# Kernel tuning notes

Measured on AMD Instinct MI355X. Metric: run time of the kernel, lower is better.

## Reference

```python
import jax, jax.numpy as jnp
import numpy as np

COUNT_PRIOR_LOG_ODDS = -2.0  # frozen value of exponential_decay(**cfg.OBJ_PRES_COUNT_LOG_PRIOR)
EPS = 1e-9                   # safe_log epsilon
B, H, W = 1024, 16, 16


def setup_inputs() -> dict:
    key = jax.random.key(0)
    k1, k2 = jax.random.split(key)
    z_pres = jax.random.uniform(k1, (B, 1, H, W), dtype=jnp.float32)
    z_pres_prob = jax.random.uniform(k2, (B, 1, H, W), dtype=jnp.float32)
    return {"z_pres": z_pres, "z_pres_prob": z_pres_prob}


def _safe_log(x):
    return jnp.log(x + EPS)


def reference(z_pres, z_pres_prob):
    b, _, h, w = z_pres.shape
    hw = h * w
    s = hw + 1  # count support size

    count_support = jnp.arange(s, dtype=jnp.float32)  # [S]
    p = 1.0 / (jnp.exp(jnp.float32(-COUNT_PRIOR_LOG_ODDS)) + 1.0)
    cd0 = (1.0 - p) * p ** count_support
    cd0 = cd0 / cd0.sum()
    cd0 = jnp.broadcast_to(cd0[None, :], (b, s))      # count_distribution [B, S]
    csf0 = jnp.zeros((b, 1), jnp.float32)             # count_so_far [B, 1]

    # flatten grid in row-major (h, w) order to scan axis: [HW, B, 1]
    probs = z_pres_prob.reshape(b, 1, hw).transpose(2, 0, 1)
    pres = z_pres.reshape(b, 1, hw).transpose(2, 0, 1)
    steps = jnp.arange(hw, dtype=jnp.float32)

    def step(carry, xs):
        cd, csf = carry                 # [B, S], [B, 1]
        prob, zp, i = xs                # [B, 1], [B, 1], scalar
        denom = hw - i
        # P(z=1 | C, z_prev): clamp(count_support - count_so_far, 0, HW - i) / (HW - i)
        p_z_given = jnp.clip(count_support[None, :] - csf, 0.0, denom) / denom  # [B, S]
        p_z = jnp.sum(cd * p_z_given, axis=1, keepdims=True)                    # [B, 1] (the bmm)
        kl = (prob * (_safe_log(prob) - _safe_log(p_z))
              + (1.0 - prob) * (_safe_log(1.0 - prob) - _safe_log(1.0 - p_z)))
        sample = jnp.round(zp)                                                  # [B, 1]
        mult = sample * p_z_given + (1.0 - sample) * (1.0 - p_z_given)          # [B, S]
        cd1 = mult * cd
        norm = jnp.clip(jnp.sum(cd1, axis=1, keepdims=True), 1e-6, None)
        return (cd1 / norm, csf + sample), kl

    (_, _), kls = jax.lax.scan(step, (cd0, csf0), (probs, pres, steps))
    # kls: [HW, B, 1] -> obj_kl [B, 1, H, W]
    return kls.transpose(1, 2, 0).reshape(b, 1, h, w)
```

## Files before the change

kernel.cpp:

```cpp
#include <hip/hip_runtime.h>
#include <math.h>

#define HW 256
#define MINNORM 1.17549435e-38f


struct InvTbl { float v[HW]; };
static constexpr InvTbl make_inv() {
    InvTbl t{};
    for (int i = 0; i < HW; ++i) t.v[i] = 1.0f / (float)(HW - i);
    return t;
}
__constant__ InvTbl INVD = make_inv();

template <int CTRL>
__device__ __forceinline__ float dpp_sra(float x) {
    int s = __builtin_amdgcn_update_dpp(0, __builtin_bit_cast(int, x),
                                        CTRL, 0xf, 0xf, true);
    return x + __builtin_bit_cast(float, s);
}

__device__ __forceinline__ float rdlane(float x, int l) {
    return __builtin_bit_cast(float,
        __builtin_amdgcn_readlane(__builtin_bit_cast(int, x), l));
}

__device__ __forceinline__ float wave_total(float x) {
    x = dpp_sra<0x111>(x);
    x = dpp_sra<0x112>(x);
    x = dpp_sra<0x114>(x);
    x = dpp_sra<0x118>(x);
    const float a = rdlane(x, 15), b = rdlane(x, 31), c = rdlane(x, 47);
    return (a + b) + c;
}

__global__ void __launch_bounds__(64)
spair_count_kl(const float* __restrict__ z_pres,
               const float* __restrict__ z_prob,
               float* __restrict__ out) {
    float tok;
    asm volatile("s_setreg_imm32_b32 hwreg(HW_REG_MODE, 4, 2), 0\n\t"
                 "v_mov_b32 %0, 0" : "=v"(tok));

    const int lane = threadIdx.x;
    const int b = blockIdx.x;

    const float e2f = (float)exp(2.0);
    const float pf  = (float)(1.0 / ((double)e2f + 1.0));
    const double pd = (double)pf;
    const double l2p = log2(pd);
    float cd = 0.0f;
    if (lane <= 41) {
        const double powj = exp2((double)lane * l2p);
        float v = (float)((1.0 - pd) * powj);
        cd = (v < MINNORM) ? 0.0f : v;
    }
    {
        float s = cd;
#pragma unroll
        for (int off = 32; off > 0; off >>= 1) s += __shfl_xor(s, off, 64);
        cd = cd / s;
    }
    cd += tok;
    const float jf = (float)lane;
    float csf = tok;

    const float* presb = z_pres + (size_t)b * HW;
    const float* probb = z_prob + (size_t)b * HW;
    float* outb = out + (size_t)b * HW;

    bool dead = false;

#pragma unroll 1
    for (int k = 0; k < 4; ++k) {
        const float myprob = probb[k * 64 + lane];
        const float mypres = presb[k * 64 + lane];
        const unsigned long long smask = __ballot(rintf(mypres) != 0.0f);
        float my_pz = 0.0f;

        if (!dead) {
#pragma unroll 1
            for (int blk = 0; blk < 4; ++blk) {
                float p2 = 1.0f;
#pragma unroll
                for (int u = 0; u < 16; ++u) {
                    const int ii = blk * 16 + u;
                    const int i = k * 64 + ii;
                    const float fden = (float)(HW - i);
                    const float inv = INVD.v[i];
                    const bool s1 = ((smask >> ii) & 1ULL) != 0ULL;

                    const float t = fminf(fmaxf(jf - csf, 0.0f), fden);
                    const float pg = (t == fden) ? 1.0f : t * inv;
                    const float mult = s1 ? pg : (1.0f - pg);

                    const float prodm = cd * mult;
                    const float p1 = cd * pg;
                    p2 = wave_total(prodm);
                    const float p1s = wave_total(p1);
                    const float pz = s1 ? p2 : p1s;

                    const float norm = fmaxf(p2, 1e-6f);
                    cd = prodm * __builtin_amdgcn_rcpf(norm);
                    csf += s1 ? 1.0f : 0.0f;

                    my_pz = (ii == lane) ? pz : my_pz;
                }
                if (p2 == 0.0f) { dead = true; break; }
            }
        }

        const float prob = myprob;
        const float pz = my_pz;
        const float kl = prob * (logf(prob + 1e-9f) - logf(pz + 1e-9f))
                       + (1.0f - prob) * (logf((1.0f - prob) + 1e-9f)
                                        - logf((1.0f - pz) + 1e-9f));
        outb[k * 64 + lane] = kl;
    }
}

extern "C" void kernel_launch(void* const* d_in, const int* in_sizes, int n_in,
                              void* d_out, int out_size, void* d_ws, size_t ws_size,
                              hipStream_t stream) {
    const float* z_pres = (const float*)d_in[0];
    const float* z_prob = (const float*)d_in[1];
    float* out = (float*)d_out;
    const int nbatch = in_sizes[0] / HW;
    spair_count_kl<<<dim3(nbatch), dim3(64), 0, stream>>>(z_pres, z_prob, out);
}
```

Baseline: 69.36 us.

## Pack four batch rows per wave with 16-lane row reductions

Each wave now processes four batch elements, one per 16-lane row. Each lane holds three count-support entries, so the 42 nonzero entries fit in 48 slots. The cross-lane sums become row-local DPP butterflies that broadcast within the row, replacing the full-wave reduction that ended in readlanes, and the two sums are interleaved. This cuts the grid to a quarter of the waves and removes the scalar readlane serialization. In exchange, each lane does more work per step, and the early-exit check now waits until all four rows are dead.

```diff
diff --git a/kernel.cpp b/kernel.cpp
--- a/kernel.cpp
+++ b/kernel.cpp
@@ -14,24 +14,26 @@
 __constant__ InvTbl INVD = make_inv();
 
 template <int CTRL>
-__device__ __forceinline__ float dpp_sra(float x) {
+__device__ __forceinline__ float dpp_add(float x) {
     int s = __builtin_amdgcn_update_dpp(0, __builtin_bit_cast(int, x),
                                         CTRL, 0xf, 0xf, true);
     return x + __builtin_bit_cast(float, s);
 }
 
-__device__ __forceinline__ float rdlane(float x, int l) {
-    return __builtin_bit_cast(float,
-        __builtin_amdgcn_readlane(__builtin_bit_cast(int, x), l));
+__device__ __forceinline__ float rowsum_bcast(float x) {
+    x = dpp_add<0xB1>(x);
+    x = dpp_add<0x4E>(x);
+    x = dpp_add<0x124>(x);
+    x = dpp_add<0x128>(x);
+    return x;
 }
-
-__device__ __forceinline__ float wave_total(float x) {
-    x = dpp_sra<0x111>(x);
-    x = dpp_sra<0x112>(x);
-    x = dpp_sra<0x114>(x);
-    x = dpp_sra<0x118>(x);
-    const float a = rdlane(x, 15), b = rdlane(x, 31), c = rdlane(x, 47);
-    return (a + b) + c;
+__device__ __forceinline__ void rowsum_bcast2(float a, float z,
+                                              float& ra, float& rz) {
+    a = dpp_add<0xB1>(a);   z = dpp_add<0xB1>(z);
+    a = dpp_add<0x4E>(a);   z = dpp_add<0x4E>(z);
+    a = dpp_add<0x124>(a);  z = dpp_add<0x124>(z);
+    a = dpp_add<0x128>(a);  z = dpp_add<0x128>(z);
+    ra = a; rz = z;
 }
 
 __global__ void __launch_bounds__(64)
@@ -43,26 +45,32 @@
                  "v_mov_b32 %0, 0" : "=v"(tok));
 
     const int lane = threadIdx.x;
-    const int b = blockIdx.x;
+    const int c = lane & 15;
+    const int b = blockIdx.x * 4 + (lane >> 4);
 
     const float e2f = (float)exp(2.0);
     const float pf  = (float)(1.0 / ((double)e2f + 1.0));
     const double pd = (double)pf;
     const double l2p = log2(pd);
-    float cd = 0.0f;
-    if (lane <= 41) {
-        const double powj = exp2((double)lane * l2p);
-        float v = (float)((1.0 - pd) * powj);
-        cd = (v < MINNORM) ? 0.0f : v;
+    float cd[3], jf[3];
+#pragma unroll
+    for (int s = 0; s < 3; ++s) {
+        const int j = c + 16 * s;
+        jf[s] = (float)j;
+        float v = 0.0f;
+        if (j <= 41) {
+            const double powj = exp2((double)j * l2p);
+            float w = (float)((1.0 - pd) * powj);
+            v = (w < MINNORM) ? 0.0f : w;
+        }
+        cd[s] = v;
     }
     {
-        float s = cd;
+        const float part = (cd[0] + cd[1]) + cd[2];
+        const float rsum = rowsum_bcast(part);
 #pragma unroll
-        for (int off = 32; off > 0; off >>= 1) s += __shfl_xor(s, off, 64);
-        cd = cd / s;
+        for (int s = 0; s < 3; ++s) cd[s] = cd[s] / rsum + tok;
     }
-    cd += tok;
-    const float jf = (float)lane;
     float csf = tok;
 
     const float* presb = z_pres + (size_t)b * HW;
@@ -73,49 +81,69 @@
 
 #pragma unroll 1
     for (int k = 0; k < 4; ++k) {
-        const float myprob = probb[k * 64 + lane];
-        const float mypres = presb[k * 64 + lane];
-        const unsigned long long smask = __ballot(rintf(mypres) != 0.0f);
-        float my_pz = 0.0f;
+        float pres_q[4], prob_q[4];
+#pragma unroll
+        for (int q = 0; q < 4; ++q) {
+            pres_q[q] = presb[k * 64 + q * 16 + c];
+            prob_q[q] = probb[k * 64 + q * 16 + c];
+        }
+        unsigned int rm[4];
+#pragma unroll
+        for (int q = 0; q < 4; ++q) {
+            const unsigned long long m = __ballot(rintf(pres_q[q]) != 0.0f);
+            rm[q] = (unsigned int)(m >> (lane & 48));
+        }
+        float pzq[4] = {0.0f, 0.0f, 0.0f, 0.0f};
 
         if (!dead) {
 #pragma unroll 1
-            for (int blk = 0; blk < 4; ++blk) {
-                float p2 = 1.0f;
+            for (int q = 0; q < 4; ++q) {
+                float lastA = 1.0f;
 #pragma unroll
-                for (int u = 0; u < 16; ++u) {
-                    const int ii = blk * 16 + u;
-                    const int i = k * 64 + ii;
+                for (int cc = 0; cc < 16; ++cc) {
+                    const int i = k * 64 + q * 16 + cc;
                     const float fden = (float)(HW - i);
                     const float inv = INVD.v[i];
-                    const bool s1 = ((smask >> ii) & 1ULL) != 0ULL;
+                    const unsigned int bit = (rm[q] >> cc) & 1u;
+                    const bool s1 = bit != 0u;
 
-                    const float t = fminf(fmaxf(jf - csf, 0.0f), fden);
-                    const float pg = (t == fden) ? 1.0f : t * inv;
-                    const float mult = s1 ? pg : (1.0f - pg);
+                    float pm[3], p1v[3];
+#pragma unroll
+                    for (int s = 0; s < 3; ++s) {
+                        const float d = jf[s] - csf;
+                        const float pg0 = fmaxf(d, 0.0f) * inv;
+                        const float pg = (d >= fden) ? 1.0f : pg0;
+                        const float mult = s1 ? pg : (1.0f - pg);
+                        pm[s]  = cd[s] * mult;
+                        p1v[s] = cd[s] * pg;
+                    }
+                    const float apart = (pm[0] + pm[1]) + pm[2];
+                    const float zpart = (p1v[0] + p1v[1]) + p1v[2];
+                    float atot, ztot;
+                    rowsum_bcast2(apart, zpart, atot, ztot);
 
-                    const float prodm = cd * mult;
-                    const float p1 = cd * pg;
-                    p2 = wave_total(prodm);
-                    const float p1s = wave_total(p1);
-                    const float pz = s1 ? p2 : p1s;
+                    const float norm = fmaxf(atot, 1e-6f);
+                    const float invn = __builtin_amdgcn_rcpf(norm);
+#pragma unroll
+                    for (int s = 0; s < 3; ++s) cd[s] = pm[s] * invn;
+                    csf += (float)bit;
 
-                    const float norm = fmaxf(p2, 1e-6f);
-                    cd = prodm * __builtin_amdgcn_rcpf(norm);
-                    csf += s1 ? 1.0f : 0.0f;
-
-                    my_pz = (ii == lane) ? pz : my_pz;
+                    pzq[q] = (cc == c) ? ztot : pzq[q];
+                    lastA = atot;
                 }
-                if (p2 == 0.0f) { dead = true; break; }
+                if (__ballot(lastA != 0.0f) == 0ULL) { dead = true; break; }
             }
         }
 
-        const float prob = myprob;
-        const float pz = my_pz;
-        const float kl = prob * (logf(prob + 1e-9f) - logf(pz + 1e-9f))
-                       + (1.0f - prob) * (logf((1.0f - prob) + 1e-9f)
-                                        - logf((1.0f - pz) + 1e-9f));
-        outb[k * 64 + lane] = kl;
+#pragma unroll
+        for (int q = 0; q < 4; ++q) {
+            const float prob = prob_q[q];
+            const float pz = pzq[q];
+            const float kl = prob * (logf(prob + 1e-9f) - logf(pz + 1e-9f))
+                           + (1.0f - prob) * (logf((1.0f - prob) + 1e-9f)
+                                            - logf((1.0f - pz) + 1e-9f));
+            outb[k * 64 + q * 16 + c] = kl;
+        }
     }
 }
 
@@ -126,5 +154,5 @@
     const float* z_prob = (const float*)d_in[1];
     float* out = (float*)d_out;
     const int nbatch = in_sizes[0] / HW;
-    spair_count_kl<<<dim3(nbatch), dim3(64), 0, stream>>>(z_pres, z_prob, out);
+    spair_count_kl<<<dim3(nbatch / 4), dim3(64), 0, stream>>>(z_pres, z_prob, out);
 }
```

Result: no change. 70.61 us (+1.8%).
